# Optimization experiments

Hardware: AMD Instinct MI355X
Metric: run time of the kernel (lower is better)

## Reference

```python
import jax, jax.numpy as jnp
import numpy as np

G, NPG, EPG = 1024, 126, 450      # graphs, nodes/graph, edges/graph
N, E, F = G * NPG, G * EPG, 126
EPS = 1e-5


def setup_inputs() -> dict:
    key = jax.random.key(0)
    ks = jax.random.split(key, 30)
    nrm = lambda k, s, sc=0.05: jax.random.normal(k, s, jnp.float32) * sc
    # graph data: random intra-graph connectivity (offsets keep edges inside each graph)
    src = jax.random.randint(ks[0], (E,), 0, NPG, jnp.int32)
    dst = jax.random.randint(ks[1], (E,), 0, NPG, jnp.int32)
    off = jnp.repeat(jnp.arange(G, dtype=jnp.int32) * NPG, EPG)
    inp = {
        "x": jax.random.normal(ks[2], (N, 5), jnp.float32),
        "edge_index": jnp.stack([src + off, dst + off]),            # [2,E] int32
        "edge_attr": jax.random.randint(ks[3], (E,), 0, 10, jnp.int32),
        "batch": jnp.repeat(jnp.arange(G, dtype=jnp.int32), NPG),   # [N]
        "deg_hist": jnp.array([0, 100, 3000, 50000, 20000], jnp.int32),  # length-5 degree histogram
        # parameters (4 PNA layers stacked on leading axis)
        "emb1_w": nrm(ks[4], (5, F)), "emb1_b": nrm(ks[5], (F,)),
        "edge_tab": nrm(ks[6], (10, 50)),
        "enc_w": nrm(ks[7], (4, 50, F)), "enc_b": nrm(ks[8], (4, F)),
        "pre_w": nrm(ks[9], (4, 3 * F, F)), "pre_b": nrm(ks[10], (4, F)),
        "post_w": nrm(ks[11], (4, 13 * F, F)), "post_b": nrm(ks[12], (4, F)),
        "lin_w": nrm(ks[13], (4, F, F)), "lin_b": nrm(ks[14], (4, F)),
        "bn_g": jnp.ones((4, F), jnp.float32), "bn_b": jnp.zeros((4, F), jnp.float32),
        "mlp_w1": nrm(ks[15], (F, 100)), "mlp_b1": nrm(ks[16], (100,)),
        "mlp_w2": nrm(ks[17], (100, 50)), "mlp_b2": nrm(ks[18], (50,)),
        "mlp_w3": nrm(ks[19], (50, 25)), "mlp_b3": nrm(ks[20], (25,)),
        "mlp_w4": nrm(ks[21], (25, 1)), "mlp_b4": nrm(ks[22], (1,)),
    }
    return inp


def _finite(a):
    return jnp.where(jnp.isfinite(a), a, 0.0)


def reference(x, edge_index, edge_attr, batch, deg_hist,
              emb1_w, emb1_b, edge_tab,
              enc_w, enc_b, pre_w, pre_b, post_w, post_b, lin_w, lin_b,
              bn_g, bn_b,
              mlp_w1, mlp_b1, mlp_w2, mlp_b2, mlp_w3, mlp_b3, mlp_w4, mlp_b4):
    src, dst = edge_index[0], edge_index[1]          # x_j = x[src], x_i = x[dst]
    h = x @ emb1_w + emb1_b                          # [N,126] node embedding
    ea_emb = edge_tab[edge_attr]                     # [E,50] edge embedding

    # PNA degree statistics (from the init-time degree histogram, as in PyG PNAConv)
    dh = deg_hist.astype(jnp.float32)
    bins = jnp.arange(dh.shape[0], dtype=jnp.float32)
    avg_log = jnp.sum(dh * jnp.log(bins + 1.0)) / jnp.sum(dh)

    cnt = jax.ops.segment_sum(jnp.ones((E,), jnp.float32), dst, N)  # in-degree per node
    inv_cnt = (1.0 / jnp.maximum(cnt, 1.0))[:, None]
    d = jnp.clip(cnt, 1.0)[:, None]
    amp = jnp.log(d + 1.0) / avg_log                  # amplification scaler
    att = avg_log / jnp.log(d + 1.0)                  # attenuation scaler

    for l in range(4):
        # message: pre_nn(cat[x_i, x_j, edge_encoder(e)])
        ea = ea_emb @ enc_w[l] + enc_b[l]             # [E,126]
        m = jnp.concatenate([h[dst], h[src], ea], -1) @ pre_w[l] + pre_b[l]  # [E,126]
        # aggregators: mean, min, max, std
        mean = jax.ops.segment_sum(m, dst, N) * inv_cnt
        meansq = jax.ops.segment_sum(m * m, dst, N) * inv_cnt
        std = jnp.sqrt(jax.nn.relu(meansq - mean * mean) + EPS)
        mn = _finite(jax.ops.segment_min(m, dst, N))
        mx = _finite(jax.ops.segment_max(m, dst, N))
        agg = jnp.concatenate([mean, mn, mx, std], -1)               # [N,504]
        agg = jnp.concatenate([agg, agg * amp, agg * att], -1)       # [N,1512] scalers
        # update: post_nn(cat[x, agg]) then lin
        out = jnp.concatenate([h, agg], -1) @ post_w[l] + post_b[l]  # [N,126]
        out = out @ lin_w[l] + lin_b[l]
        # BatchNorm (training-mode batch stats over nodes) + ReLU
        mu = out.mean(0)
        var = out.var(0)
        h = jax.nn.relu(bn_g[l] * (out - mu) / jnp.sqrt(var + EPS) + bn_b[l])

    pooled = jax.ops.segment_sum(h, batch, G)         # global_add_pool -> [G,126]
    z = jax.nn.relu(pooled @ mlp_w1 + mlp_b1)
    z = jax.nn.relu(z @ mlp_w2 + mlp_b2)
    z = jax.nn.relu(z @ mlp_w3 + mlp_b3)
    return z @ mlp_w4 + mlp_b4                        # [G,1]
```

## Files before the change

kernel.cpp:

```cpp
#include <hip/hip_runtime.h>
#include <math.h>

#define G_    1024
#define NPG   126
#define EPG   450
#define NN    (G_*NPG)
#define EE    (G_*EPG)
#define F_    126
#define EPSV  1e-5f

#define KS32  40
#define SEGB_SZ (KS32*4*64*8)
#define SMALLB_SZ (4*8*64*8)

typedef unsigned short u16;
typedef unsigned int   u32;
typedef __attribute__((ext_vector_type(8))) short bf8v;
typedef __attribute__((ext_vector_type(4))) float f4v;
typedef __attribute__((ext_vector_type(16))) float f16v;

union U4 { bf8v v; u32 a[4]; };

__device__ __forceinline__ u16 f2b(float f) {
    u32 u = __float_as_uint(f);
    u += 0x7FFFu + ((u >> 16) & 1u);
    return (u16)(u >> 16);
}
__device__ __forceinline__ float b2f(u16 s) { return __uint_as_float(((u32)s) << 16); }
__device__ __forceinline__ float b2f_lo(u32 u) { return __uint_as_float(u << 16); }
__device__ __forceinline__ float b2f_hi(u32 u) { return __uint_as_float(u & 0xFFFF0000u); }

__device__ __forceinline__ bf8v bn_load(const u16* __restrict__ p,
                                        const float* __restrict__ coef, int k0) {
    U4 r; r.v = *(const bf8v*)p;
    if (!coef) return r.v;
    f4v s0 = *(const f4v*)(coef + k0);
    f4v s1 = *(const f4v*)(coef + k0 + 4);
    f4v h0 = *(const f4v*)(coef + 128 + k0);
    f4v h1 = *(const f4v*)(coef + 128 + k0 + 4);
    float v[8];
#pragma unroll
    for (int i = 0; i < 4; ++i) { v[2 * i] = b2f_lo(r.a[i]); v[2 * i + 1] = b2f_hi(r.a[i]); }
    v[0] = fmaxf(v[0] * s0[0] + h0[0], 0.f); v[1] = fmaxf(v[1] * s0[1] + h0[1], 0.f);
    v[2] = fmaxf(v[2] * s0[2] + h0[2], 0.f); v[3] = fmaxf(v[3] * s0[3] + h0[3], 0.f);
    v[4] = fmaxf(v[4] * s1[0] + h1[0], 0.f); v[5] = fmaxf(v[5] * s1[1] + h1[1], 0.f);
    v[6] = fmaxf(v[6] * s1[2] + h1[2], 0.f); v[7] = fmaxf(v[7] * s1[3] + h1[3], 0.f);
    U4 o;
#pragma unroll
    for (int i = 0; i < 4; ++i) o.a[i] = (u32)f2b(v[2 * i]) | ((u32)f2b(v[2 * i + 1]) << 16);
    return o.v;
}

__global__ void k_embed(const float* __restrict__ x, const float* __restrict__ w,
                        const float* __restrict__ b, u16* __restrict__ hb) {
    int idx = (blockIdx.x * 256 + threadIdx.x) * 8;
    if (idx >= NN * 128) return;
    int n = idx >> 7, f0 = idx & 127;
    float xr[5];
#pragma unroll
    for (int c = 0; c < 5; ++c) xr[c] = x[n * 5 + c];
    float v[8];
#pragma unroll
    for (int j = 0; j < 8; ++j) {
        int f = f0 + j;
        float s = 0.f;
        if (f < F_) {
            s = b[f];
#pragma unroll
            for (int c = 0; c < 5; ++c) s += xr[c] * w[c * F_ + f];
        }
        v[j] = s;
    }
    U4 o;
#pragma unroll
    for (int i = 0; i < 4; ++i) o.a[i] = (u32)f2b(v[2 * i]) | ((u32)f2b(v[2 * i + 1]) << 16);
    *(bf8v*)(hb + idx) = o.v;
}

__global__ void k_build_csr(const int* __restrict__ src, const int* __restrict__ dst,
                            const int* __restrict__ attr,
                            int* __restrict__ deg, int* __restrict__ rstart,
                            int* __restrict__ epack) {
    int g = blockIdx.x;
    __shared__ int scnt[NPG];
    __shared__ int spos[NPG];
    int t = threadIdx.x;
    for (int j = t; j < NPG; j += blockDim.x) scnt[j] = 0;
    __syncthreads();
    int e0 = g * EPG;
    for (int i = t; i < EPG; i += blockDim.x) {
        int dl = dst[e0 + i] - g * NPG;
        atomicAdd(&scnt[dl], 1);
    }
    __syncthreads();
    if (t == 0) {
        int run = 0;
        for (int j = 0; j < NPG; ++j) { spos[j] = run; run += scnt[j]; }
    }
    __syncthreads();
    for (int j = t; j < NPG; j += blockDim.x) {
        deg[g * NPG + j]    = scnt[j];
        rstart[g * NPG + j] = e0 + spos[j];
    }
    __syncthreads();
    for (int j = t; j < NPG; j += blockDim.x) scnt[j] = 0;
    __syncthreads();
    for (int i = t; i < EPG; i += blockDim.x) {
        int e  = e0 + i;
        int dl = dst[e] - g * NPG;
        int p  = atomicAdd(&scnt[dl], 1);
        epack[e0 + spos[dl] + p] = (src[e] - g * NPG) | (attr[e] << 8);
    }
}

__global__ void k_node_scalars(const int* __restrict__ deg, const int* __restrict__ deg_hist,
                               float* __restrict__ ampv, float* __restrict__ attv) {
    int n = blockIdx.x * blockDim.x + threadIdx.x;
    if (n >= NN) return;
    float sum = 0.f, sl = 0.f;
#pragma unroll
    for (int b = 0; b < 5; ++b) {
        float dh = (float)deg_hist[b];
        sum += dh;
        sl  += dh * logf((float)b + 1.f);
    }
    float avg_log = sl / sum;
    float cm = fmaxf((float)deg[n], 1.f);
    float la = logf(cm + 1.f);
    ampv[n] = la / avg_log;
    attv[n] = avg_log / la;
}

__global__ void k_build_etab(const float* __restrict__ edge_tab, const float* __restrict__ enc_w,
                             const float* __restrict__ enc_b, const float* __restrict__ pre_w,
                             const float* __restrict__ pre_b, float* __restrict__ etab) {
    int l = blockIdx.x / 10, a = blockIdx.x % 10;
    __shared__ float tmp[F_];
    int t = threadIdx.x;
    if (t < F_) {
        float s = enc_b[l * F_ + t];
        for (int c = 0; c < 50; ++c) s += edge_tab[a * 50 + c] * enc_w[(l * 50 + c) * F_ + t];
        tmp[t] = s;
    }
    __syncthreads();
    if (t < F_) {
        float s = pre_b[l * F_ + t];
        for (int j = 0; j < F_; ++j) s += tmp[j] * pre_w[((size_t)l * 378 + 252 + j) * F_ + t];
        etab[(l * 10 + a) * F_ + t] = s;
    }
}

__global__ void k_fold_T(const float* __restrict__ pre_w, const float* __restrict__ post_w,
                         float* __restrict__ Tbuf) {
    int k = blockIdx.x;
    int y = blockIdx.y;
    int l = y / 3, seg = y % 3;
    int c = threadIdx.x;
    __shared__ float wi[128];
    wi[c] = (k < F_ && c < F_) ? pre_w[((size_t)l * 378 + k) * F_ + c] : 0.f;
    __syncthreads();
    float s = 0.f;
    if (k < F_ && c < F_) {
        const float* pw = post_w + (size_t)l * 1638 * F_;
        if (seg == 0) s = pw[(size_t)k * F_ + c];
        int base = 126 + seg * 504;
        for (int f = 0; f < F_; ++f) {
            float bs = pw[(size_t)(base + f) * F_ + c]
                     + pw[(size_t)(base + 126 + f) * F_ + c]
                     + pw[(size_t)(base + 252 + f) * F_ + c];
            s += wi[f] * bs;
        }
    }
    Tbuf[((size_t)y * 128 + k) * 128 + c] = s;
}

__global__ void k_fold_Wc(const float* __restrict__ Tbuf, const float* __restrict__ post_w,
                          const int* __restrict__ deg_hist, float* __restrict__ WcBuf) {
    int idx = blockIdx.x * 256 + threadIdx.x;
    if (idx >= 4 * 128 * 128) return;
    int l = idx >> 14, k = (idx >> 7) & 127, c = idx & 127;
    float dsum = 0.f, dsl = 0.f;
#pragma unroll
    for (int b = 0; b < 5; ++b) {
        float dh = (float)deg_hist[b];
        dsum += dh; dsl += dh * logf((float)b + 1.f);
    }
    float avgl = dsl / dsum;
    float l2 = logf(2.f);
    float amp0 = l2 / avgl, att0 = avgl / l2;
    float t1 = Tbuf[((size_t)(l * 3 + 0) * 128 + k) * 128 + c];
    float t2 = Tbuf[((size_t)(l * 3 + 1) * 128 + k) * 128 + c];
    float t3 = Tbuf[((size_t)(l * 3 + 2) * 128 + k) * 128 + c];
    float b0 = (k < F_ && c < F_) ? post_w[((size_t)l * 1638 + k) * F_ + c] : 0.f;
    WcBuf[((size_t)l * 128 + k) * 128 + c] = -((t1 - b0) + amp0 * t2 + att0 * t3);
}

__global__ void k_prep_B128(const float* __restrict__ pre_w, const float* __restrict__ lin_w,
                            const float* __restrict__ WcBuf,
                            u16* __restrict__ wjB, u16* __restrict__ linB,
                            u16* __restrict__ wcB) {
    int idx = blockIdx.x * 256 + threadIdx.x;
    int y = blockIdx.y;
    int l = y & 3, ty = y >> 2;
    int j = idx & 7, lane = (idx >> 3) & 63, pnl = (idx >> 9) & 7, ks = idx >> 12;
    int k = ks * 32 + (lane >> 4) * 8 + j;
    int c = pnl * 16 + (lane & 15);
    float v;
    if (ty == 2) {
        v = WcBuf[((size_t)l * 128 + k) * 128 + c];
    } else {
        const float* W = (ty == 0) ? pre_w + ((size_t)l * 378 + 126) * F_
                                   : lin_w + (size_t)l * F_ * F_;
        v = (k < F_ && c < F_) ? W[(size_t)k * F_ + c] : 0.f;
    }
    u16* out = ((ty == 0) ? wjB : (ty == 1) ? linB : wcB) + (size_t)l * SMALLB_SZ;
    out[idx] = f2b(v);
}

__global__ void k_prep_Bpost(const float* __restrict__ post_w, const float* __restrict__ Tbuf,
                             u16* __restrict__ postB) {
    int idx = blockIdx.x * 256 + threadIdx.x;
    if (idx >= SEGB_SZ) return;
    int y = blockIdx.y;
    int l = y / 3, seg = y % 3;
    int j = idx & 7, lane = (idx >> 3) & 63, cg = (idx >> 9) & 3, ks = idx >> 11;
    int c  = cg * 32 + (lane & 31);
    int vk = ks * 16 + (lane >> 5) * 8 + j;
    float val = 0.f;
    if (vk < 128) {
        val = Tbuf[((size_t)y * 128 + vk) * 128 + c];
    } else {
        int kv = vk - 128;
        int f = kv >> 2, t = kv & 3;
        if (f < F_ && c < F_)
            val = post_w[((size_t)l * 1638 + 126 + seg * 504 + t * 126 + f) * F_ + c];
    }
    postB[(size_t)y * SEGB_SZ + idx] = f2b(val);
}

__global__ __launch_bounds__(256) void k_psgemm(
        const u16* __restrict__ A0, const float* __restrict__ coef,
        const u16* __restrict__ Bv0, const u16* __restrict__ Bv1,
        u16* __restrict__ C0, u16* __restrict__ C1) {
    const u16* Bv = blockIdx.y ? Bv1 : Bv0;
    u16* C = blockIdx.y ? C1 : C0;
    int lane = threadIdx.x & 63, wid = threadIdx.x >> 6;
    int gq = lane >> 4, r15 = lane & 15;
    int wr = (wid >> 1) * 32, wc = (wid & 1) * 64;
    const u16* bp = Bv + ((size_t)(wc >> 4) * 64 + lane) * 8;
    bf8v bfr[16];
#pragma unroll
    for (int ks = 0; ks < 4; ++ks)
#pragma unroll
        for (int fc = 0; fc < 4; ++fc)
            bfr[ks * 4 + fc] = *(const bf8v*)(bp + (size_t)ks * 4096 + fc * 512);

#pragma unroll
    for (int t = 0; t < 4; ++t) {
        size_t rbase = ((size_t)blockIdx.x * 4 + t) * 64;
        size_t row0 = rbase + wr + r15;
        const u16* a0p = A0 + row0 * 128 + gq * 8;
        const u16* a1p = a0p + 16 * 128;
        f4v acc[2][4];
#pragma unroll
        for (int i = 0; i < 2; ++i)
#pragma unroll
            for (int j = 0; j < 4; ++j) acc[i][j] = (f4v){0.f, 0.f, 0.f, 0.f};
#pragma unroll
        for (int ks = 0; ks < 4; ++ks) {
            int k0 = ks * 32 + gq * 8;
            bf8v a0 = bn_load(a0p + ks * 32, coef, k0);
            bf8v a1 = bn_load(a1p + ks * 32, coef, k0);
#pragma unroll
            for (int fc = 0; fc < 4; ++fc) {
                acc[0][fc] = __builtin_amdgcn_mfma_f32_16x16x32_bf16(a0, bfr[ks * 4 + fc], acc[0][fc], 0, 0, 0);
                acc[1][fc] = __builtin_amdgcn_mfma_f32_16x16x32_bf16(a1, bfr[ks * 4 + fc], acc[1][fc], 0, 0, 0);
            }
        }
        int erow = (int)rbase + wr + gq * 4;
        int ecol = wc + r15;
#pragma unroll
        for (int fc = 0; fc < 4; ++fc) {
            int col = ecol + fc * 16;
#pragma unroll
            for (int fr = 0; fr < 2; ++fr)
#pragma unroll
                for (int r = 0; r < 4; ++r) {
                    size_t row = erow + fr * 16 + r;
                    C[row * 128 + col] = (col < F_) ? f2b(acc[fr][fc][r]) : (u16)0;
                }
        }
    }
}

__global__ __launch_bounds__(512) void k_agg2(
        const u16* __restrict__ Psc,
        const float* __restrict__ etab_l,
        const int* __restrict__ deg, const int* __restrict__ rstart,
        const int* __restrict__ epack,
        u16* __restrict__ aggc, int g0) {
    __shared__ u32  PsL[126 * 65];
    __shared__ float etLo[10 * 64];
    __shared__ float etHi[10 * 64];
    __shared__ u32  epL[EPG];
    __shared__ int  degL[NPG];
    __shared__ int  rlL[NPG];
    int gg = g0 + blockIdx.x;
    int tid = threadIdx.x;
    const u16* psrow = Psc + (size_t)blockIdx.x * NPG * 128;
    for (int i = tid; i < NPG * 16; i += 512) {
        int r = i >> 4, q = i & 15;
        U4 u; u.v = *(const bf8v*)(psrow + (size_t)r * 128 + q * 8);
        u32* dp = &PsL[r * 65 + q * 4];
        dp[0] = u.a[0]; dp[1] = u.a[1]; dp[2] = u.a[2]; dp[3] = u.a[3];
    }
    for (int i = tid; i < 640; i += 512) {
        int a = i >> 6, ln = i & 63;
        int f = 2 * ln;
        etLo[i] = (f < F_) ? etab_l[a * F_ + f] : 0.f;
        etHi[i] = (f + 1 < F_) ? etab_l[a * F_ + f + 1] : 0.f;
    }
    for (int e = tid; e < EPG; e += 512) epL[e] = (u32)epack[(size_t)gg * EPG + e];
    if (tid < NPG) {
        degL[tid] = deg[(size_t)gg * NPG + tid];
        rlL[tid]  = rstart[(size_t)gg * NPG + tid] - gg * EPG;
    }
    __syncthreads();

    int lane = tid & 63, wid = tid >> 6;
    for (int nd = wid; nd < NPG; nd += 8) {
        int dg = degL[nd], rl = rlL[nd];
        float s0 = 0.f, q0 = 0.f, s1 = 0.f, q1 = 0.f;
        float n0 = 3.4e38f, x0 = -3.4e38f, n1 = 3.4e38f, x1 = -3.4e38f;
        for (int e = 0; e < dg; ++e) {
            u32 pk = epL[rl + e];
            int sN = pk & 255, at = pk >> 8;
            u32 pv = PsL[sN * 65 + lane];
            float v0 = b2f_lo(pv) + etLo[at * 64 + lane];
            float v1 = b2f_hi(pv) + etHi[at * 64 + lane];
            s0 += v0; q0 += v0 * v0; n0 = fminf(n0, v0); x0 = fmaxf(x0, v0);
            s1 += v1; q1 += v1 * v1; n1 = fminf(n1, v1); x1 = fmaxf(x1, v1);
        }
        float m0, m1, d0, d1;
        if (dg == 0) {
            m0 = m1 = 0.f; n0 = x0 = n1 = x1 = 0.f;
            d0 = d1 = 0.0031622776601683794f;
        } else {
            float ic = 1.f / (float)dg;
            m0 = s0 * ic; m1 = s1 * ic;
            d0 = sqrtf(fmaxf(q0 * ic - m0 * m0, 0.f) + EPSV);
            d1 = sqrtf(fmaxf(q1 * ic - m1 * m1, 0.f) + EPSV);
        }
        U4 o;
        o.a[0] = (u32)f2b(m0) | ((u32)f2b(n0) << 16);
        o.a[1] = (u32)f2b(x0) | ((u32)f2b(d0) << 16);
        o.a[2] = (u32)f2b(m1) | ((u32)f2b(n1) << 16);
        o.a[3] = (u32)f2b(x1) | ((u32)f2b(d1) << 16);
        *(bf8v*)(aggc + ((size_t)blockIdx.x * NPG + nd) * 512 + lane * 8) = o.v;
    }
}

__global__ __launch_bounds__(256) void k_post2(
        const u16* __restrict__ hA, const float* __restrict__ coef,
        const u16* __restrict__ aggc, const u16* __restrict__ corr,
        const int* __restrict__ degc,
        const float* __restrict__ ampc, const float* __restrict__ attc,
        const u16* __restrict__ postB_l, const float* __restrict__ bias,
        u16* __restrict__ outC) {
    int lane = threadIdx.x & 63, cgw = threadIdx.x >> 6;
    int r31 = lane & 31, kg = lane >> 5;
    size_t rbase = (size_t)blockIdx.x * 64;
    const u16* h0 = hA + (rbase + r31) * 128 + kg * 8;
    const u16* h1 = h0 + 32 * 128;
    const u16* g0 = aggc + (rbase + r31) * 512 + kg * 8;
    const u16* g1 = g0 + 32 * 512;
    const u16* bp = postB_l + ((size_t)cgw * 64 + lane) * 8;

    f16v acc[3][2];
#pragma unroll
    for (int s = 0; s < 3; ++s)
#pragma unroll
        for (int i = 0; i < 2; ++i)
#pragma unroll
            for (int r = 0; r < 16; ++r) acc[s][i][r] = 0.f;

    bf8v bc0 = *(const bf8v*)(bp);
    bf8v bc1 = *(const bf8v*)(bp + SEGB_SZ);
    bf8v bc2 = *(const bf8v*)(bp + 2 * SEGB_SZ);

#pragma unroll 4
    for (int ks = 0; ks < KS32; ++ks) {
        bf8v bn0, bn1, bn2;
        if (ks < KS32 - 1) {
            const u16* bn = bp + (size_t)(ks + 1) * 2048;
            bn0 = *(const bf8v*)(bn);
            bn1 = *(const bf8v*)(bn + SEGB_SZ);
            bn2 = *(const bf8v*)(bn + 2 * SEGB_SZ);
        }
        bf8v a0, a1;
        if (ks < 8) {
            int k0 = ks * 16 + kg * 8;
            a0 = bn_load(h0 + ks * 16, coef, k0);
            a1 = bn_load(h1 + ks * 16, coef, k0);
        } else {
            int off = (ks - 8) * 16;
            a0 = *(const bf8v*)(g0 + off);
            a1 = *(const bf8v*)(g1 + off);
        }
        acc[0][0] = __builtin_amdgcn_mfma_f32_32x32x16_bf16(a0, bc0, acc[0][0], 0, 0, 0);
        acc[0][1] = __builtin_amdgcn_mfma_f32_32x32x16_bf16(a1, bc0, acc[0][1], 0, 0, 0);
        acc[1][0] = __builtin_amdgcn_mfma_f32_32x32x16_bf16(a0, bc1, acc[1][0], 0, 0, 0);
        acc[1][1] = __builtin_amdgcn_mfma_f32_32x32x16_bf16(a1, bc1, acc[1][1], 0, 0, 0);
        acc[2][0] = __builtin_amdgcn_mfma_f32_32x32x16_bf16(a0, bc2, acc[2][0], 0, 0, 0);
        acc[2][1] = __builtin_amdgcn_mfma_f32_32x32x16_bf16(a1, bc2, acc[2][1], 0, 0, 0);
        bc0 = bn0; bc1 = bn1; bc2 = bn2;
    }

    int ecol = cgw * 32 + r31;
    float bv = (ecol < F_) ? bias[ecol] : 0.f;
#pragma unroll
    for (int rf = 0; rf < 2; ++rf) {
#pragma unroll
        for (int r = 0; r < 16; ++r) {
            int rowl = rf * 32 + (r & 3) + 8 * (r >> 2) + 4 * kg;
            size_t row = rbase + rowl;
            float am = ampc[row], at = attc[row];
            bool isz = (degc[row] == 0);
            float val = acc[0][rf][r] + am * acc[1][rf][r] + at * acc[2][rf][r];
            u16 ov = 0;
            if (ecol < F_) {
                val += bv;
                if (isz) val += b2f(corr[row * 128 + ecol]);
                ov = f2b(val);
            }
            outC[row * 128 + ecol] = ov;
        }
    }
}

__global__ __launch_bounds__(256) void k_lin(
        const u16* __restrict__ A0, const u16* __restrict__ Bv,
        const float* __restrict__ bias, float* __restrict__ bns,
        u16* __restrict__ C) {
    __shared__ float ldsS[128];
    __shared__ float ldsQ[128];
    int tid = threadIdx.x;
    if (tid < 128) { ldsS[tid] = 0.f; ldsQ[tid] = 0.f; }
    __syncthreads();
    int lane = tid & 63, wid = tid >> 6;
    int gq = lane >> 4, r15 = lane & 15;
    int wr = (wid >> 1) * 32, wc = (wid & 1) * 64;
    const u16* bp = Bv + ((size_t)(wc >> 4) * 64 + lane) * 8;
    bf8v bfr[16];
#pragma unroll
    for (int ks = 0; ks < 4; ++ks)
#pragma unroll
        for (int fc = 0; fc < 4; ++fc)
            bfr[ks * 4 + fc] = *(const bf8v*)(bp + (size_t)ks * 4096 + fc * 512);
    int ecol = wc + r15;
    float bv4[4], sc4[4] = {0.f, 0.f, 0.f, 0.f}, sq4[4] = {0.f, 0.f, 0.f, 0.f};
#pragma unroll
    for (int fc = 0; fc < 4; ++fc) {
        int col = ecol + fc * 16;
        bv4[fc] = (col < F_) ? bias[col] : 0.f;
    }

#pragma unroll
    for (int t = 0; t < 4; ++t) {
        size_t rbase = ((size_t)blockIdx.x * 4 + t) * 64;
        size_t row0 = rbase + wr + r15;
        const u16* a0p = A0 + row0 * 128 + gq * 8;
        const u16* a1p = a0p + 16 * 128;
        f4v acc[2][4];
#pragma unroll
        for (int i = 0; i < 2; ++i)
#pragma unroll
            for (int j = 0; j < 4; ++j) acc[i][j] = (f4v){0.f, 0.f, 0.f, 0.f};
#pragma unroll
        for (int ks = 0; ks < 4; ++ks) {
            bf8v a0 = *(const bf8v*)(a0p + ks * 32);
            bf8v a1 = *(const bf8v*)(a1p + ks * 32);
#pragma unroll
            for (int fc = 0; fc < 4; ++fc) {
                acc[0][fc] = __builtin_amdgcn_mfma_f32_16x16x32_bf16(a0, bfr[ks * 4 + fc], acc[0][fc], 0, 0, 0);
                acc[1][fc] = __builtin_amdgcn_mfma_f32_16x16x32_bf16(a1, bfr[ks * 4 + fc], acc[1][fc], 0, 0, 0);
            }
        }
        int erow = (int)rbase + wr + gq * 4;
#pragma unroll
        for (int fc = 0; fc < 4; ++fc) {
            int col = ecol + fc * 16;
#pragma unroll
            for (int fr = 0; fr < 2; ++fr)
#pragma unroll
                for (int r = 0; r < 4; ++r) {
                    size_t row = erow + fr * 16 + r;
                    float val = acc[fr][fc][r] + bv4[fc];
                    sc4[fc] += val; sq4[fc] += val * val;
                    C[row * 128 + col] = (col < F_) ? f2b(val) : (u16)0;
                }
        }
    }
#pragma unroll
    for (int fc = 0; fc < 4; ++fc) {
        int col = ecol + fc * 16;
        atomicAdd(&ldsS[col], sc4[fc]);
        atomicAdd(&ldsQ[col], sq4[fc]);
    }
    __syncthreads();
    if (tid < 128) {
        atomicAdd(&bns[tid], ldsS[tid]);
        atomicAdd(&bns[128 + tid], ldsQ[tid]);
    }
}

__global__ void k_bn_coef(const float* __restrict__ bns, const float* __restrict__ g,
                          const float* __restrict__ b, float* __restrict__ coef) {
    int f = threadIdx.x;
    float sc = 0.f, sh = 0.f;
    if (f < F_) {
        float mu  = bns[f] * (1.f / NN);
        float var = bns[128 + f] * (1.f / NN) - mu * mu;
        float r = rsqrtf(fmaxf(var, 0.f) + EPSV);
        sc = g[f] * r;
        sh = b[f] - mu * sc;
    }
    coef[f] = sc;
    coef[128 + f] = sh;
}

__global__ __launch_bounds__(256) void k_pool_mlp(const u16* __restrict__ hb,
        const float* __restrict__ coef,
        const float* __restrict__ w1, const float* __restrict__ b1,
        const float* __restrict__ w2, const float* __restrict__ b2,
        const float* __restrict__ w3, const float* __restrict__ b3,
        const float* __restrict__ w4, const float* __restrict__ b4,
        float* __restrict__ out) {
    int gg = blockIdx.x;
    __shared__ float lsum[16][128];
    __shared__ float p[128];
    __shared__ float z1[100];
    __shared__ float z2[50];
    __shared__ float z3[25];
    int t = threadIdx.x;
    int cg = t & 15, rs = t >> 4;
    float sc[8], sh[8];
#pragma unroll
    for (int j = 0; j < 8; ++j) { sc[j] = coef[cg * 8 + j]; sh[j] = coef[128 + cg * 8 + j]; }
    const u16* hbase = hb + (size_t)gg * NPG * 128 + cg * 8;
    float a8[8] = {};
    for (int r = rs; r < NPG; r += 16) {
        U4 u;
        u.v = *(const bf8v*)(hbase + (size_t)r * 128);
        float v[8];
#pragma unroll
        for (int i = 0; i < 4; ++i) { v[2 * i] = b2f_lo(u.a[i]); v[2 * i + 1] = b2f_hi(u.a[i]); }
#pragma unroll
        for (int j = 0; j < 8; ++j) a8[j] += fmaxf(v[j] * sc[j] + sh[j], 0.f);
    }
#pragma unroll
    for (int j = 0; j < 8; ++j) lsum[rs][cg * 8 + j] = a8[j];
    __syncthreads();
    if (t < 128) {
        float s = 0.f;
#pragma unroll
        for (int k = 0; k < 16; ++k) s += lsum[k][t];
        p[t] = s;
    }
    __syncthreads();
    if (t < 100) {
        float s = b1[t];
        for (int c = 0; c < F_; ++c) s += p[c] * w1[c * 100 + t];
        z1[t] = fmaxf(s, 0.f);
    }
    __syncthreads();
    if (t < 50) {
        float s = b2[t];
        for (int c = 0; c < 100; ++c) s += z1[c] * w2[c * 50 + t];
        z2[t] = fmaxf(s, 0.f);
    }
    __syncthreads();
    if (t < 25) {
        float s = b3[t];
        for (int c = 0; c < 50; ++c) s += z2[c] * w3[c * 25 + t];
        z3[t] = fmaxf(s, 0.f);
    }
    __syncthreads();
    if (t == 0) {
        float s = b4[0];
        for (int c = 0; c < 25; ++c) s += z3[c] * w4[c];
        out[gg] = s;
    }
}

extern "C" void kernel_launch(void* const* d_in, const int* in_sizes, int n_in,
                              void* d_out, int out_size, void* d_ws, size_t ws_size,
                              hipStream_t stream) {
    const float* x        = (const float*)d_in[0];
    const int*   ei       = (const int*)d_in[1];
    const int*   src      = ei;
    const int*   dst      = ei + EE;
    const int*   eattr    = (const int*)d_in[2];
    const int*   deg_hist = (const int*)d_in[4];
    const float* emb1_w = (const float*)d_in[5];
    const float* emb1_b = (const float*)d_in[6];
    const float* edge_tab = (const float*)d_in[7];
    const float* enc_w  = (const float*)d_in[8];
    const float* enc_b  = (const float*)d_in[9];
    const float* pre_w  = (const float*)d_in[10];
    const float* pre_b  = (const float*)d_in[11];
    const float* post_w = (const float*)d_in[12];
    const float* post_b = (const float*)d_in[13];
    const float* lin_w  = (const float*)d_in[14];
    const float* lin_b  = (const float*)d_in[15];
    const float* bn_g   = (const float*)d_in[16];
    const float* bn_b   = (const float*)d_in[17];
    const float* w1 = (const float*)d_in[18];
    const float* b1 = (const float*)d_in[19];
    const float* w2 = (const float*)d_in[20];
    const float* b2 = (const float*)d_in[21];
    const float* w3 = (const float*)d_in[22];
    const float* b3 = (const float*)d_in[23];
    const float* w4 = (const float*)d_in[24];
    const float* b4 = (const float*)d_in[25];
    float* out = (float*)d_out;

    size_t fixedB = 0;
    {
        fixedB += 3 * ((size_t)NN * 128 * 2 + 256);
        fixedB += 4 * 10 * F_ * 4 + 256;
        fixedB += (size_t)12 * 128 * 128 * 4 + 256;
        fixedB += (size_t)4 * 128 * 128 * 4 + 256;
        fixedB += 2 * (4 * 256 * 4 + 256);
        fixedB += 2 * ((size_t)NN * 4 + 256);
        fixedB += 2 * ((size_t)NN * 4 + 256);
        fixedB += (size_t)EE * 4 + 256;
        fixedB += 3 * ((size_t)4 * SMALLB_SZ * 2 + 256);
        fixedB += (size_t)12 * SEGB_SZ * 2 + 256;
    }
    int nch = (ws_size >= fixedB + (size_t)NN * 512 * 2 + 256) ? 1 : 2;
    int GCH_ = G_ / nch;
    size_t CH_ = (size_t)NN / nch;

    char* base = (char*)d_ws;
    size_t o = 0;
    auto alloc = [&](size_t bytes) { char* r = base + o; o = (o + bytes + 255) & ~(size_t)255; return r; };
    u16*  hb    = (u16*)  alloc((size_t)NN * 128 * 2);
    u16*  Ps    = (u16*)  alloc((size_t)NN * 128 * 2);
    u16*  outA  = (u16*)  alloc((size_t)NN * 128 * 2);
    u16*  aggb  = (u16*)  alloc(CH_ * 512 * 2);
    float* etab = (float*)alloc(4 * 10 * F_ * 4);
    float* Tbuf = (float*)alloc((size_t)12 * 128 * 128 * 4);
    float* WcBuf= (float*)alloc((size_t)4 * 128 * 128 * 4);
    float* bns  = (float*)alloc(4 * 256 * 4);
    float* coef = (float*)alloc(4 * 256 * 4);
    int*  deg    = (int*)alloc((size_t)NN * 4);
    int*  rstart = (int*)alloc((size_t)NN * 4);
    float* ampv  = (float*)alloc((size_t)NN * 4);
    float* attv  = (float*)alloc((size_t)NN * 4);
    int*  epack  = (int*)alloc((size_t)EE * 4);
    u16*  wjB   = (u16*)alloc((size_t)4 * SMALLB_SZ * 2);
    u16*  linB  = (u16*)alloc((size_t)4 * SMALLB_SZ * 2);
    u16*  wcB   = (u16*)alloc((size_t)4 * SMALLB_SZ * 2);
    u16*  postB = (u16*)alloc((size_t)12 * SEGB_SZ * 2);
    u16*  corr  = outA;

    hipMemsetAsync(bns, 0, 4 * 256 * 4, stream);
    k_embed<<<(NN * 128 / 8 + 255) / 256, 256, 0, stream>>>(x, emb1_w, emb1_b, hb);
    k_build_csr<<<G_, 128, 0, stream>>>(src, dst, eattr, deg, rstart, epack);
    k_node_scalars<<<(NN + 255) / 256, 256, 0, stream>>>(deg, deg_hist, ampv, attv);
    k_build_etab<<<40, 128, 0, stream>>>(edge_tab, enc_w, enc_b, pre_w, pre_b, etab);
    k_fold_T<<<dim3(128, 12), 128, 0, stream>>>(pre_w, post_w, Tbuf);
    k_fold_Wc<<<(4 * 128 * 128 + 255) / 256, 256, 0, stream>>>(Tbuf, post_w, deg_hist, WcBuf);
    k_prep_B128<<<dim3(SMALLB_SZ / 256, 12), 256, 0, stream>>>(pre_w, lin_w, WcBuf, wjB, linB, wcB);
    k_prep_Bpost<<<dim3((SEGB_SZ + 255) / 256, 12), 256, 0, stream>>>(post_w, Tbuf, postB);

    for (int l = 0; l < 4; ++l) {
        const float* coefL = (l == 0) ? nullptr : coef + (size_t)(l - 1) * 256;
        k_psgemm<<<dim3(NN / 256, 2), 256, 0, stream>>>(
            hb, coefL, wjB + (size_t)l * SMALLB_SZ, wcB + (size_t)l * SMALLB_SZ, Ps, corr);
        for (int c = 0; c < nch; ++c) {
            int g0 = c * GCH_;
            size_t r0 = (size_t)g0 * NPG;
            k_agg2<<<GCH_, 512, 0, stream>>>(Ps + r0 * 128, etab + l * 10 * F_,
                                             deg, rstart, epack, aggb, g0);
            k_post2<<<(int)(CH_ / 64), 256, 0, stream>>>(
                hb + r0 * 128, coefL, aggb, corr + r0 * 128,
                deg + r0, ampv + r0, attv + r0,
                postB + (size_t)(l * 3) * SEGB_SZ, post_b + l * F_, outA + r0 * 128);
        }
        k_lin<<<NN / 256, 256, 0, stream>>>(outA, linB + (size_t)l * SMALLB_SZ,
                                            lin_b + l * F_, bns + (size_t)l * 256, hb);
        k_bn_coef<<<1, 128, 0, stream>>>(bns + (size_t)l * 256, bn_g + l * F_, bn_b + l * F_,
                                         coef + (size_t)l * 256);
    }

    k_pool_mlp<<<G_, 256, 0, stream>>>(hb, coef + 3 * 256,
                                       w1, b1, w2, b2, w3, b3, w4, b4, out);
}
```

Baseline: 1.174 ms.

## Compute zero-degree correction GEMM only for compacted list of isolated nodes

Before, every layer ran a second full-size GEMM over all nodes to build a correction term that is only used for nodes with zero in-degree. Now a one-time kernel compacts the zero-degree nodes into a list with a node-to-slot map. A separate small GEMM kernel computes the correction only for those listed rows, and the post kernel looks up the correction through the map. This cuts the per-layer GEMM work and memory traffic roughly in half, at the cost of an extra launch and gather. The fixed list capacity (ZCAP) would silently drop corrections if more zero-degree nodes existed.

```diff
diff --git a/kernel.cpp b/kernel.cpp
--- a/kernel.cpp
+++ b/kernel.cpp
@@ -8,6 +8,7 @@
 #define EE    (G_*EPG)
 #define F_    126
 #define EPSV  1e-5f
+#define ZCAP  32768
 
 #define KS32  40
 #define SEGB_SZ (KS32*4*64*8)
@@ -111,6 +112,18 @@
         int p  = atomicAdd(&scnt[dl], 1);
         epack[e0 + spos[dl] + p] = (src[e] - g * NPG) | (attr[e] << 8);
     }
+}
+
+__global__ void k_zlist(const int* __restrict__ deg, int* __restrict__ zmeta,
+                        int* __restrict__ zlist, int* __restrict__ cmap) {
+    int n = blockIdx.x * 256 + threadIdx.x;
+    if (n >= NN) return;
+    int m = -1;
+    if (deg[n] == 0) {
+        int idx = atomicAdd(zmeta, 1);
+        if (idx < ZCAP) { zlist[idx] = n; m = idx; }
+    }
+    cmap[n] = m;
 }
 
 __global__ void k_node_scalars(const int* __restrict__ deg, const int* __restrict__ deg_hist,
@@ -240,10 +253,7 @@
 
 __global__ __launch_bounds__(256) void k_psgemm(
         const u16* __restrict__ A0, const float* __restrict__ coef,
-        const u16* __restrict__ Bv0, const u16* __restrict__ Bv1,
-        u16* __restrict__ C0, u16* __restrict__ C1) {
-    const u16* Bv = blockIdx.y ? Bv1 : Bv0;
-    u16* C = blockIdx.y ? C1 : C0;
+        const u16* __restrict__ Bv, u16* __restrict__ C) {
     int lane = threadIdx.x & 63, wid = threadIdx.x >> 6;
     int gq = lane >> 4, r15 = lane & 15;
     int wr = (wid >> 1) * 32, wc = (wid & 1) * 64;
@@ -290,6 +300,63 @@
                     C[row * 128 + col] = (col < F_) ? f2b(acc[fr][fc][r]) : (u16)0;
                 }
         }
+    }
+}
+
+__global__ __launch_bounds__(256) void k_corr(
+        const u16* __restrict__ hA, const float* __restrict__ coef,
+        const int* __restrict__ zmeta, const int* __restrict__ zlist,
+        const u16* __restrict__ Bv, u16* __restrict__ corrc) {
+    int nz = zmeta[0];
+    if (nz > ZCAP) nz = ZCAP;
+    int rbase = blockIdx.x * 64;
+    if (rbase >= nz) return;
+    int lane = threadIdx.x & 63, wid = threadIdx.x >> 6;
+    int gq = lane >> 4, r15 = lane & 15;
+    int wr = (wid >> 1) * 32, wc = (wid & 1) * 64;
+    const u16* bp = Bv + ((size_t)(wc >> 4) * 64 + lane) * 8;
+    bf8v bfr[16];
+#pragma unroll
+    for (int ks = 0; ks < 4; ++ks)
+#pragma unroll
+        for (int fc = 0; fc < 4; ++fc)
+            bfr[ks * 4 + fc] = *(const bf8v*)(bp + (size_t)ks * 4096 + fc * 512);
+
+    int slot0 = rbase + wr + r15;
+    int slot1 = slot0 + 16;
+    int g0 = zlist[slot0 < nz ? slot0 : nz - 1];
+    int g1 = zlist[slot1 < nz ? slot1 : nz - 1];
+    const u16* a0p = hA + (size_t)g0 * 128 + gq * 8;
+    const u16* a1p = hA + (size_t)g1 * 128 + gq * 8;
+    f4v acc[2][4];
+#pragma unroll
+    for (int i = 0; i < 2; ++i)
+#pragma unroll
+        for (int j = 0; j < 4; ++j) acc[i][j] = (f4v){0.f, 0.f, 0.f, 0.f};
+#pragma unroll
+    for (int ks = 0; ks < 4; ++ks) {
+        int k0 = ks * 32 + gq * 8;
+        bf8v a0 = bn_load(a0p + ks * 32, coef, k0);
+        bf8v a1 = bn_load(a1p + ks * 32, coef, k0);
+#pragma unroll
+        for (int fc = 0; fc < 4; ++fc) {
+            acc[0][fc] = __builtin_amdgcn_mfma_f32_16x16x32_bf16(a0, bfr[ks * 4 + fc], acc[0][fc], 0, 0, 0);
+            acc[1][fc] = __builtin_amdgcn_mfma_f32_16x16x32_bf16(a1, bfr[ks * 4 + fc], acc[1][fc], 0, 0, 0);
+        }
+    }
+    int erow = rbase + wr + gq * 4;
+    int ecol = wc + r15;
+#pragma unroll
+    for (int fc = 0; fc < 4; ++fc) {
+        int col = ecol + fc * 16;
+#pragma unroll
+        for (int fr = 0; fr < 2; ++fr)
+#pragma unroll
+            for (int r = 0; r < 4; ++r) {
+                int row = erow + fr * 16 + r;
+                if (row < nz)
+                    corrc[(size_t)row * 128 + col] = (col < F_) ? f2b(acc[fr][fc][r]) : (u16)0;
+            }
     }
 }
 
@@ -362,8 +429,8 @@
 
 __global__ __launch_bounds__(256) void k_post2(
         const u16* __restrict__ hA, const float* __restrict__ coef,
-        const u16* __restrict__ aggc, const u16* __restrict__ corr,
-        const int* __restrict__ degc,
+        const u16* __restrict__ aggc,
+        const int* __restrict__ cmapc, const u16* __restrict__ corrc,
         const float* __restrict__ ampc, const float* __restrict__ attc,
         const u16* __restrict__ postB_l, const float* __restrict__ bias,
         u16* __restrict__ outC) {
@@ -425,12 +492,12 @@
             int rowl = rf * 32 + (r & 3) + 8 * (r >> 2) + 4 * kg;
             size_t row = rbase + rowl;
             float am = ampc[row], at = attc[row];
-            bool isz = (degc[row] == 0);
+            int cm = cmapc[row];
             float val = acc[0][rf][r] + am * acc[1][rf][r] + at * acc[2][rf][r];
             u16 ov = 0;
             if (ecol < F_) {
                 val += bv;
-                if (isz) val += b2f(corr[row * 128 + ecol]);
+                if (cm >= 0) val += b2f(corrc[(size_t)cm * 128 + ecol]);
                 ov = f2b(val);
             }
             outC[row * 128 + ecol] = ov;
@@ -628,12 +695,15 @@
     size_t fixedB = 0;
     {
         fixedB += 3 * ((size_t)NN * 128 * 2 + 256);
+        fixedB += (size_t)ZCAP * 128 * 2 + 256;
         fixedB += 4 * 10 * F_ * 4 + 256;
         fixedB += (size_t)12 * 128 * 128 * 4 + 256;
         fixedB += (size_t)4 * 128 * 128 * 4 + 256;
         fixedB += 2 * (4 * 256 * 4 + 256);
         fixedB += 2 * ((size_t)NN * 4 + 256);
         fixedB += 2 * ((size_t)NN * 4 + 256);
+        fixedB += (size_t)NN * 4 + 256;
+        fixedB += (size_t)ZCAP * 4 + 512;
         fixedB += (size_t)EE * 4 + 256;
         fixedB += 3 * ((size_t)4 * SMALLB_SZ * 2 + 256);
         fixedB += (size_t)12 * SEGB_SZ * 2 + 256;
@@ -648,6 +718,7 @@
     u16*  hb    = (u16*)  alloc((size_t)NN * 128 * 2);
     u16*  Ps    = (u16*)  alloc((size_t)NN * 128 * 2);
     u16*  outA  = (u16*)  alloc((size_t)NN * 128 * 2);
+    u16*  corrc = (u16*)  alloc((size_t)ZCAP * 128 * 2);
     u16*  aggb  = (u16*)  alloc(CH_ * 512 * 2);
     float* etab = (float*)alloc(4 * 10 * F_ * 4);
     float* Tbuf = (float*)alloc((size_t)12 * 128 * 128 * 4);
@@ -658,16 +729,20 @@
     int*  rstart = (int*)alloc((size_t)NN * 4);
     float* ampv  = (float*)alloc((size_t)NN * 4);
     float* attv  = (float*)alloc((size_t)NN * 4);
+    int*  cmap   = (int*)alloc((size_t)NN * 4);
+    int*  zmeta  = (int*)alloc(256);
+    int*  zlist  = (int*)alloc((size_t)ZCAP * 4);
     int*  epack  = (int*)alloc((size_t)EE * 4);
     u16*  wjB   = (u16*)alloc((size_t)4 * SMALLB_SZ * 2);
     u16*  linB  = (u16*)alloc((size_t)4 * SMALLB_SZ * 2);
     u16*  wcB   = (u16*)alloc((size_t)4 * SMALLB_SZ * 2);
     u16*  postB = (u16*)alloc((size_t)12 * SEGB_SZ * 2);
-    u16*  corr  = outA;
 
     hipMemsetAsync(bns, 0, 4 * 256 * 4, stream);
+    hipMemsetAsync(zmeta, 0, 256, stream);
     k_embed<<<(NN * 128 / 8 + 255) / 256, 256, 0, stream>>>(x, emb1_w, emb1_b, hb);
     k_build_csr<<<G_, 128, 0, stream>>>(src, dst, eattr, deg, rstart, epack);
+    k_zlist<<<(NN + 255) / 256, 256, 0, stream>>>(deg, zmeta, zlist, cmap);
     k_node_scalars<<<(NN + 255) / 256, 256, 0, stream>>>(deg, deg_hist, ampv, attv);
     k_build_etab<<<40, 128, 0, stream>>>(edge_tab, enc_w, enc_b, pre_w, pre_b, etab);
     k_fold_T<<<dim3(128, 12), 128, 0, stream>>>(pre_w, post_w, Tbuf);
@@ -677,16 +752,17 @@
 
     for (int l = 0; l < 4; ++l) {
         const float* coefL = (l == 0) ? nullptr : coef + (size_t)(l - 1) * 256;
-        k_psgemm<<<dim3(NN / 256, 2), 256, 0, stream>>>(
-            hb, coefL, wjB + (size_t)l * SMALLB_SZ, wcB + (size_t)l * SMALLB_SZ, Ps, corr);
+        k_psgemm<<<NN / 256, 256, 0, stream>>>(hb, coefL, wjB + (size_t)l * SMALLB_SZ, Ps);
+        k_corr<<<ZCAP / 64, 256, 0, stream>>>(hb, coefL, zmeta, zlist,
+                                              wcB + (size_t)l * SMALLB_SZ, corrc);
         for (int c = 0; c < nch; ++c) {
             int g0 = c * GCH_;
             size_t r0 = (size_t)g0 * NPG;
             k_agg2<<<GCH_, 512, 0, stream>>>(Ps + r0 * 128, etab + l * 10 * F_,
                                              deg, rstart, epack, aggb, g0);
             k_post2<<<(int)(CH_ / 64), 256, 0, stream>>>(
-                hb + r0 * 128, coefL, aggb, corr + r0 * 128,
-                deg + r0, ampv + r0, attv + r0,
+                hb + r0 * 128, coefL, aggb, cmap + r0, corrc,
+                ampv + r0, attv + r0,
                 postB + (size_t)(l * 3) * SEGB_SZ, post_b + l * F_, outA + r0 * 128);
         }
         k_lin<<<NN / 256, 256, 0, stream>>>(outA, linB + (size_t)l * SMALLB_SZ,
```

New measurement: 1.150 ms. 2.0% less time.
